# Performance work log

Hardware: AMD Instinct MI355X
Metric: run time of the kernel (lower is better)

## Reference

```python
import jax, jax.numpy as jnp
import numpy as np

D = 512
H = 8
DH = D // H
DFF = 2048
SLOTS = 1024
TOPK = 5
LN_EPS = 1e-5
NORM_EPS = 1e-12


def setup_inputs() -> dict:
    key = jax.random.key(0)
    ks = jax.random.split(key, 12)
    B, S = 8, 1024
    inp = {
        "src": jax.random.normal(ks[0], (B, S, D), dtype=jnp.float32),
        # MultiheadAttention params (torch layout: in_proj [3D, D], out_proj [D, D])
        "in_proj_w": jax.random.normal(ks[1], (3 * D, D), dtype=jnp.float32) * 0.02,
        "in_proj_b": jnp.zeros((3 * D,), dtype=jnp.float32),
        "out_proj_w": jax.random.normal(ks[2], (D, D), dtype=jnp.float32) * 0.02,
        "out_proj_b": jnp.zeros((D,), dtype=jnp.float32),
        # BPBookMemory params
        "memory": jax.random.normal(ks[3], (SLOTS, D), dtype=jnp.float32),
        "retrieval_scale": jnp.asarray(0.1, dtype=jnp.float32),
        # LayerNorms
        "ln1_g": jnp.ones((D,), dtype=jnp.float32),
        "ln1_b": jnp.zeros((D,), dtype=jnp.float32),
        "ln2_g": jnp.ones((D,), dtype=jnp.float32),
        "ln2_b": jnp.zeros((D,), dtype=jnp.float32),
        # FFN (torch Linear layout: [out, in])
        "w1": jax.random.normal(ks[4], (DFF, D), dtype=jnp.float32) * 0.02,
        "b1": jnp.zeros((DFF,), dtype=jnp.float32),
        "w2": jax.random.normal(ks[5], (D, DFF), dtype=jnp.float32) * 0.02,
        "b2": jnp.zeros((D,), dtype=jnp.float32),
    }
    return inp


def _layer_norm(x, g, b):
    mu = jnp.mean(x, axis=-1, keepdims=True)
    var = jnp.var(x, axis=-1, keepdims=True)
    return (x - mu) * jax.lax.rsqrt(var + LN_EPS) * g + b


def _l2_normalize(x):
    n = jnp.linalg.norm(x, axis=-1, keepdims=True)
    return x / jnp.maximum(n, NORM_EPS)


def _forward(src, in_proj_w, in_proj_b, out_proj_w, out_proj_b,
             memory, retrieval_scale, ln1_g, ln1_b, ln2_g, ln2_b,
             w1, b1, w2, b2):
    B, S, _ = src.shape
    # ---- pre-norm self-attention ----
    h = _layer_norm(src, ln1_g, ln1_b)
    qkv = h @ in_proj_w.T + in_proj_b            # [B,S,3D]
    q, k, v = jnp.split(qkv, 3, axis=-1)
    q = q.reshape(B, S, H, DH)
    k = k.reshape(B, S, H, DH)
    v = v.reshape(B, S, H, DH)
    scores = jnp.einsum("bqhd,bkhd->bhqk", q, k) / jnp.sqrt(jnp.float32(DH))
    attn = jax.nn.softmax(scores, axis=-1)
    ctx = jnp.einsum("bhqk,bkhd->bqhd", attn, v).reshape(B, S, D)
    attn_out = ctx @ out_proj_w.T + out_proj_b
    src = src + attn_out
    # ---- BP-Book memory: cosine sim -> topk -> softmax -> gather -> weighted sum ----
    xn = _l2_normalize(src)                      # [B,S,D]
    mn = _l2_normalize(memory)                   # [SLOTS,D]
    sim = xn @ mn.T                              # [B,S,SLOTS]
    topk_scores, topk_idx = jax.lax.top_k(sim, TOPK)
    w = jax.nn.softmax(topk_scores, axis=-1)     # [B,S,TOPK]
    retrieved = memory[topk_idx]                 # [B,S,TOPK,D]
    weighted = jnp.einsum("bskd,bsk->bsd", retrieved, w)
    src = src + retrieval_scale * weighted
    # ---- FFN ----
    h = _layer_norm(src, ln2_g, ln2_b)
    ffn = jax.nn.gelu(h @ w1.T + b1, approximate=False) @ w2.T + b2
    return src + ffn


def reference(src, in_proj_w, in_proj_b, out_proj_w, out_proj_b,
              memory, retrieval_scale, ln1_g, ln1_b, ln2_g, ln2_b,
              w1, b1, w2, b2):
    return _forward(src, in_proj_w, in_proj_b, out_proj_w, out_proj_b,
                    memory, retrieval_scale, ln1_g, ln1_b, ln2_g, ln2_b,
                    w1, b1, w2, b2)
```

## Files before the change

### kernel.cpp

```cpp
#include <hip/hip_runtime.h>
#include <math.h>

#define D_ 512
#define H_ 8
#define DFF_ 2048
#define SLOTS_ 1024
#define TOPK_ 5
#define NCAND_ 8
#define NTOK_ 8192
#define SEQ_ 1024
#define LN_EPS_ 1e-5f

typedef __attribute__((ext_vector_type(8))) short bf16x8;
typedef __attribute__((ext_vector_type(4))) float f32x4;
typedef __attribute__((ext_vector_type(4))) unsigned u32x4;
typedef unsigned short u16;

__device__ inline void split2(float x, unsigned short& hi, unsigned short& lo) {
    unsigned u = __builtin_bit_cast(unsigned, x);
    hi = (unsigned short)(u >> 16);
    float h = __builtin_bit_cast(float, u & 0xFFFF0000u);
    float rem = x - h;
    lo = (unsigned short)(__builtin_bit_cast(unsigned, rem) >> 16);
}

__device__ __forceinline__ void gld16(const void* g, void* l) {
    __builtin_amdgcn_global_load_lds(
        (const __attribute__((address_space(1))) void*)g,
        (__attribute__((address_space(3))) void*)l, 16, 0, 0);
}

__device__ __forceinline__ int SW7(int r) { return (r ^ (r >> 3)) & 7; }
__device__ __forceinline__ const bf16x8* frag(const unsigned short* p, int r, int c) {
    return (const bf16x8*)(p + r * 64 + ((c ^ SW7(r)) << 3));
}

__global__ __launch_bounds__(256) void prep_kernel(
    const float* __restrict__ inw, const float* __restrict__ outw,
    const float* __restrict__ w1, const float* __restrict__ w2,
    const float* __restrict__ mem, const float* __restrict__ src,
    const float* __restrict__ ln1g, const float* __restrict__ ln1b,
    u16* __restrict__ inwh, u16* __restrict__ inwl,
    u16* __restrict__ outwh, u16* __restrict__ outwl,
    u16* __restrict__ w1h, u16* __restrict__ w2h,
    float* __restrict__ mn, u16* __restrict__ mnh, u16* __restrict__ mnl,
    u16* __restrict__ hh, u16* __restrict__ hl)
{
    const int bid = blockIdx.x;
    const int t = threadIdx.x;
    if (bid < 3072) {
        const int i = (bid * 256 + t) * 4;
        const float* x;
        u16 *hhp, *llp;
        int base;
        if (i < 786432)       { x = inw;  hhp = inwh;  llp = inwl;  base = 0; }
        else if (i < 1048576) { x = outw; hhp = outwh; llp = outwl; base = 786432; }
        else if (i < 2097152) { x = w1;   hhp = w1h;   llp = nullptr; base = 1048576; }
        else                  { x = w2;   hhp = w2h;   llp = nullptr; base = 2097152; }
        const int j = i - base;
        const float4 v = *(const float4*)(x + j);
        const float vv[4] = {v.x, v.y, v.z, v.w};
        u16 h[4], l[4];
#pragma unroll
        for (int e = 0; e < 4; ++e) split2(vv[e], h[e], l[e]);
        hhp[j + 0] = h[0]; hhp[j + 1] = h[1]; hhp[j + 2] = h[2]; hhp[j + 3] = h[3];
        if (llp) { llp[j + 0] = l[0]; llp[j + 1] = l[1]; llp[j + 2] = l[2]; llp[j + 3] = l[3]; }
    } else if (bid < 3328) {
        const int row = (bid - 3072) * 4 + (t >> 6);
        const int lane = t & 63;
        float v[8];
        float ss = 0.0f;
#pragma unroll
        for (int j = 0; j < 8; ++j) {
            v[j] = mem[(size_t)row * D_ + j * 64 + lane];
            ss += v[j] * v[j];
        }
#pragma unroll
        for (int off = 32; off; off >>= 1) ss += __shfl_xor(ss, off);
        const float inv = 1.0f / fmaxf(sqrtf(ss), 1e-12f);
#pragma unroll
        for (int j = 0; j < 8; ++j) {
            const float y = v[j] * inv;
            mn[(size_t)row * D_ + j * 64 + lane] = y;
            u16 h, l;
            split2(y, h, l);
            mnh[(size_t)row * D_ + j * 64 + lane] = h;
            mnl[(size_t)row * D_ + j * 64 + lane] = l;
        }
    } else {
        const int row = bid - 3328;
        const float a = src[(size_t)row * D_ + t];
        const float b = src[(size_t)row * D_ + t + 256];
        float s = a + b;
        float ss = a * a + b * b;
#pragma unroll
        for (int off = 32; off; off >>= 1) {
            s += __shfl_xor(s, off);
            ss += __shfl_xor(ss, off);
        }
        __shared__ float rs[4], rss[4];
        if ((t & 63) == 0) { rs[t >> 6] = s; rss[t >> 6] = ss; }
        __syncthreads();
        s = rs[0] + rs[1] + rs[2] + rs[3];
        ss = rss[0] + rss[1] + rss[2] + rss[3];
        const float mu = s * (1.0f / D_);
        const float var = ss * (1.0f / D_) - mu * mu;
        const float r = rsqrtf(var + LN_EPS_);
        const float y0 = (a - mu) * r * ln1g[t] + ln1b[t];
        const float y1 = (b - mu) * r * ln1g[t + 256] + ln1b[t + 256];
        u16 h0, l0, h1, l1;
        split2(y0, h0, l0);
        split2(y1, h1, l1);
        hh[(size_t)row * D_ + t] = h0;
        hh[(size_t)row * D_ + t + 256] = h1;
        hl[(size_t)row * D_ + t] = l0;
        hl[(size_t)row * D_ + t + 256] = l1;
    }
}

enum { EP_QKV = 0, EP_OUTPROJ = 1, EP_SIM = 2, EP_FFN1 = 3, EP_FFN2 = 4 };

template <int SPLIT, int MODE>
__global__ __launch_bounds__(256) void gemm_mf(
    const unsigned short* __restrict__ Ahg, const unsigned short* __restrict__ Alg,
    const unsigned short* __restrict__ Bhg, const unsigned short* __restrict__ Blg,
    const float* __restrict__ bias, const float* __restrict__ res,
    float* __restrict__ C,
    unsigned short* __restrict__ Ch, unsigned short* __restrict__ Cl,
    int M, int N, int K)
{
    __shared__ __align__(16) unsigned short sm[(SPLIT == 3 ? 4 : 2) * 8192];
    unsigned short* Ah = sm;
    unsigned short* Al = sm + 8192;
    unsigned short* Bh = sm + (SPLIT == 3 ? 16384 : 8192);
    unsigned short* Bl = sm + 24576;

    const int tid = threadIdx.x;
    const int lane = tid & 63;
    const int w = tid >> 6;
    const int wr = w >> 1, wc = w & 1;
    const int g = lane >> 4, ln = lane & 15;
    const int m0 = blockIdx.x * 128, n0 = blockIdx.y * 128;
    const int lrow8 = lane >> 3, lchunk = lane & 7;

    const unsigned short* gsrc;
    unsigned short* lds;
    int rbase, rofs, nblk;
    if (SPLIT == 3) {
        nblk = 16; rofs = 0;
        if (w == 0)      { gsrc = Ahg; lds = Ah; rbase = m0; }
        else if (w == 1) { gsrc = Alg; lds = Al; rbase = m0; }
        else if (w == 2) { gsrc = Bhg; lds = Bh; rbase = n0; }
        else             { gsrc = Blg; lds = Bl; rbase = n0; }
    } else {
        nblk = 8; rofs = (w & 1) * 64;
        if (w < 2) { gsrc = Ahg; lds = Ah; rbase = m0; }
        else       { gsrc = Bhg; lds = Bh; rbase = n0; }
    }

    f32x4 acc[4][4];
#pragma unroll
    for (int i = 0; i < 4; ++i)
#pragma unroll
        for (int j = 0; j < 4; ++j) acc[i][j] = (f32x4){0.f, 0.f, 0.f, 0.f};

    for (int k0 = 0; k0 < K; k0 += 64) {
#pragma unroll
        for (int blk = 0; blk < nblk; ++blk) {
            const int row = rofs + blk * 8 + lrow8;
            const int sc = lchunk ^ SW7(row);
            gld16(gsrc + (size_t)(rbase + row) * K + k0 + sc * 8,
                  lds + (rofs + blk * 8) * 64);
        }
        __syncthreads();

#pragma unroll
        for (int ks = 0; ks < 2; ++ks) {
            bf16x8 a_h[4], a_l[4], b_h[4], b_l[4];
#pragma unroll
            for (int mi = 0; mi < 4; ++mi) {
                a_h[mi] = *frag(Ah, wr * 64 + mi * 16 + ln, ks * 4 + g);
                if (SPLIT == 3) a_l[mi] = *frag(Al, wr * 64 + mi * 16 + ln, ks * 4 + g);
            }
#pragma unroll
            for (int ni = 0; ni < 4; ++ni) {
                b_h[ni] = *frag(Bh, wc * 64 + ni * 16 + ln, ks * 4 + g);
                if (SPLIT == 3) b_l[ni] = *frag(Bl, wc * 64 + ni * 16 + ln, ks * 4 + g);
            }
#pragma unroll
            for (int mi = 0; mi < 4; ++mi)
#pragma unroll
                for (int ni = 0; ni < 4; ++ni) {
                    acc[mi][ni] = __builtin_amdgcn_mfma_f32_16x16x32_bf16(
                        a_h[mi], b_h[ni], acc[mi][ni], 0, 0, 0);
                    if (SPLIT == 3) {
                        acc[mi][ni] = __builtin_amdgcn_mfma_f32_16x16x32_bf16(
                            a_h[mi], b_l[ni], acc[mi][ni], 0, 0, 0);
                        acc[mi][ni] = __builtin_amdgcn_mfma_f32_16x16x32_bf16(
                            a_l[mi], b_h[ni], acc[mi][ni], 0, 0, 0);
                    }
                }
        }
        __syncthreads();
    }

#pragma unroll
    for (int mi = 0; mi < 4; ++mi) {
#pragma unroll
        for (int ni = 0; ni < 4; ++ni) {
            const int gn = n0 + wc * 64 + ni * 16 + ln;
            const float bz = (MODE == EP_SIM) ? 0.0f : bias[gn];
#pragma unroll
            for (int r2 = 0; r2 < 4; ++r2) {
                const int gm = m0 + wr * 64 + mi * 16 + g * 4 + r2;
                float v = acc[mi][ni][r2];
                if (MODE == EP_SIM) {
                    unsigned short h16, l16;
                    split2(v, h16, l16);
                    Ch[(size_t)gm * N + gn] = h16;
                } else if (MODE == EP_QKV) {
                    v += bz;
                    if (gn < D_) v *= 0.125f;
                    unsigned short h16, l16;
                    split2(v, h16, l16);
                    Ch[(size_t)gm * N + gn] = h16;
                    Cl[(size_t)gm * N + gn] = l16;
                } else if (MODE == EP_OUTPROJ) {
                    v += bz + res[(size_t)gm * N + gn];
                    C[(size_t)gm * N + gn] = v;
                    unsigned short h16, l16;
                    split2(v, h16, l16);
                    Ch[(size_t)gm * N + gn] = h16;
                } else if (MODE == EP_FFN1) {
                    v += bz;
                    v = 0.5f * v * (1.0f + erff(v * 0.70710678118654752f));
                    unsigned short h16, l16;
                    split2(v, h16, l16);
                    Ch[(size_t)gm * N + gn] = h16;
                } else {
                    v += bz + res[(size_t)gm * N + gn];
                    C[(size_t)gm * N + gn] = v;
                }
            }
        }
    }
}

__global__ __launch_bounds__(256, 2) void attn_kernel(
    const unsigned short* __restrict__ qkvh, const unsigned short* __restrict__ qkvl,
    unsigned short* __restrict__ ctxh, unsigned short* __restrict__ ctxl)
{
    const int id = blockIdx.x;
    const int bh = id & 63;
    const int qt = id >> 6;
    const int b = bh >> 3, h = bh & 7;
    const int tok0 = b * SEQ_ + qt * 128;
    const int kbase0 = b * SEQ_;
    const int tid = threadIdx.x;
    const int lane = tid & 63;
    const int w = tid >> 6;
    const int ln = lane & 15, g = lane >> 4;
    const int lrow8 = lane >> 3, lchunk = lane & 7;

    __shared__ __align__(16) unsigned char smb[65536];
    unsigned*       PP  = (unsigned*)smb;
    unsigned short* Qh  = (unsigned short*)smb;
    unsigned short* Ql  = (unsigned short*)(smb + 16384);
    unsigned short* Kh  = (unsigned short*)(smb + 32768);
    unsigned short* Kl  = (unsigned short*)(smb + 40960);
    unsigned short* Vth = (unsigned short*)(smb + 49152);
    unsigned short* Vtl = (unsigned short*)(smb + 57344);

    const int qoff = h * 64, koff = 512 + h * 64, voff = 1024 + h * 64;

#pragma unroll
    for (int blk = 0; blk < 4; ++blk) {
        const int row = w * 32 + blk * 8 + lrow8;
        const int sc = lchunk ^ SW7(row);
        gld16(qkvh + (size_t)(tok0 + row) * 1536 + qoff + sc * 8,
              Qh + (w * 32 + blk * 8) * 64);
        gld16(qkvl + (size_t)(tok0 + row) * 1536 + qoff + sc * 8,
              Ql + (w * 32 + blk * 8) * 64);
    }
    __syncthreads();
    bf16x8 qfh[2][2], qfl[2][2];
#pragma unroll
    for (int qi = 0; qi < 2; ++qi)
#pragma unroll
        for (int ks = 0; ks < 2; ++ks) {
            qfh[qi][ks] = *frag(Qh, w * 32 + qi * 16 + ln, ks * 4 + g);
            qfl[qi][ks] = *frag(Ql, w * 32 + qi * 16 + ln, ks * 4 + g);
        }
    __syncthreads();

    f32x4 o[4][2];
#pragma unroll
    for (int di = 0; di < 4; ++di)
#pragma unroll
        for (int qi = 0; qi < 2; ++qi) o[di][qi] = (f32x4){0.f, 0.f, 0.f, 0.f};
    float mrow2[2] = {-INFINITY, -INFINITY};
    float lrow2[2] = {0.f, 0.f};

    const int p2 = tid & 31, dc = tid >> 5;

    for (int kt = 0; kt < 16; ++kt) {
        const int kb2 = kbase0 + kt * 64;
#pragma unroll
        for (int blk = 0; blk < 2; ++blk) {
            const int row = w * 16 + blk * 8 + lrow8;
            const int sc = lchunk ^ SW7(row);
            gld16(qkvh + (size_t)(kb2 + row) * 1536 + koff + sc * 8,
                  Kh + (w * 16 + blk * 8) * 64);
            gld16(qkvl + (size_t)(kb2 + row) * 1536 + koff + sc * 8,
                  Kl + (w * 16 + blk * 8) * 64);
        }
        {
            const size_t b0 = (size_t)(kb2 + 2 * p2) * 1536 + voff + dc * 8;
            const bf16x8 h0 = *(const bf16x8*)(qkvh + b0);
            const bf16x8 h1 = *(const bf16x8*)(qkvh + b0 + 1536);
            const bf16x8 l0 = *(const bf16x8*)(qkvl + b0);
            const bf16x8 l1 = *(const bf16x8*)(qkvl + b0 + 1536);
#pragma unroll
            for (int j = 0; j < 8; ++j) {
                const int d = dc * 8 + j;
                const int idx = d * 64 + (((p2 >> 2) ^ SW7(d)) << 3) + ((p2 & 3) << 1);
                *(unsigned*)&Vth[idx] = (unsigned)(unsigned short)h0[j]
                                      | ((unsigned)(unsigned short)h1[j] << 16);
                *(unsigned*)&Vtl[idx] = (unsigned)(unsigned short)l0[j]
                                      | ((unsigned)(unsigned short)l1[j] << 16);
            }
        }
        __syncthreads();

        f32x4 s[4][2];
#pragma unroll
        for (int ki = 0; ki < 4; ++ki)
#pragma unroll
            for (int qi = 0; qi < 2; ++qi) s[ki][qi] = (f32x4){0.f, 0.f, 0.f, 0.f};
        __builtin_amdgcn_s_setprio(1);
#pragma unroll
        for (int ks = 0; ks < 2; ++ks) {
            bf16x8 kbh[4], kbl[4];
#pragma unroll
            for (int ki = 0; ki < 4; ++ki) {
                kbh[ki] = *frag(Kh, ki * 16 + ln, ks * 4 + g);
                kbl[ki] = *frag(Kl, ki * 16 + ln, ks * 4 + g);
            }
#pragma unroll
            for (int ki = 0; ki < 4; ++ki)
#pragma unroll
                for (int qi = 0; qi < 2; ++qi) {
                    s[ki][qi] = __builtin_amdgcn_mfma_f32_16x16x32_bf16(kbh[ki], qfh[qi][ks], s[ki][qi], 0, 0, 0);
                    s[ki][qi] = __builtin_amdgcn_mfma_f32_16x16x32_bf16(kbh[ki], qfl[qi][ks], s[ki][qi], 0, 0, 0);
                    s[ki][qi] = __builtin_amdgcn_mfma_f32_16x16x32_bf16(kbl[ki], qfh[qi][ks], s[ki][qi], 0, 0, 0);
                }
        }
        __builtin_amdgcn_s_setprio(0);

        float tm2[2], alpha2[2], psum2[2];
#pragma unroll
        for (int qi = 0; qi < 2; ++qi) {
            float m01 = fmaxf(fmaxf(s[0][qi][0], s[0][qi][1]), fmaxf(s[0][qi][2], s[0][qi][3]));
            float m23 = fmaxf(fmaxf(s[1][qi][0], s[1][qi][1]), fmaxf(s[1][qi][2], s[1][qi][3]));
            float m45 = fmaxf(fmaxf(s[2][qi][0], s[2][qi][1]), fmaxf(s[2][qi][2], s[2][qi][3]));
            float m67 = fmaxf(fmaxf(s[3][qi][0], s[3][qi][1]), fmaxf(s[3][qi][2], s[3][qi][3]));
            tm2[qi] = fmaxf(fmaxf(m01, m23), fmaxf(m45, m67));
        }
#pragma unroll
        for (int qi = 0; qi < 2; ++qi) {
            tm2[qi] = fmaxf(tm2[qi], __shfl_xor(tm2[qi], 16));
            tm2[qi] = fmaxf(tm2[qi], __shfl_xor(tm2[qi], 32));
            const float mnew = fmaxf(mrow2[qi], tm2[qi]);
            alpha2[qi] = __expf(mrow2[qi] - mnew);
            mrow2[qi] = mnew;
            psum2[qi] = 0.f;
        }
#pragma unroll
        for (int qi = 0; qi < 2; ++qi)
#pragma unroll
            for (int ki = 0; ki < 4; ++ki) {
                u32x4 pv;
#pragma unroll
                for (int r2 = 0; r2 < 4; ++r2) {
                    const float p = __expf(s[ki][qi][r2] - mrow2[qi]);
                    psum2[qi] += p;
                    unsigned short h16, l16;
                    split2(p, h16, l16);
                    pv[r2] = (unsigned)h16 | ((unsigned)l16 << 16);
                }
                *(u32x4*)&PP[(w * 32 + qi * 16 + ln) * 64 + (((ki * 4 + g) ^ (ln & 7)) << 2)] = pv;
            }
#pragma unroll
        for (int qi = 0; qi < 2; ++qi) {
            psum2[qi] += __shfl_xor(psum2[qi], 16);
            psum2[qi] += __shfl_xor(psum2[qi], 32);
            lrow2[qi] = lrow2[qi] * alpha2[qi] + psum2[qi];
        }
#pragma unroll
        for (int di = 0; di < 4; ++di)
#pragma unroll
            for (int qi = 0; qi < 2; ++qi)
#pragma unroll
                for (int r2 = 0; r2 < 4; ++r2)
                    o[di][qi][r2] *= alpha2[qi];

        __builtin_amdgcn_s_setprio(1);
#pragma unroll
        for (int ks = 0; ks < 2; ++ks) {
            bf16x8 pah[2], pal[2];
#pragma unroll
            for (int qi = 0; qi < 2; ++qi) {
                const unsigned* rowp = PP + (w * 32 + qi * 16 + ln) * 64;
                const int c0 = (2 * ks + (g >> 1)) * 4 + (g & 1) * 2;
                const u32x4 q0 = *(const u32x4*)(rowp + (((c0    ) ^ (ln & 7)) << 2));
                const u32x4 q1 = *(const u32x4*)(rowp + (((c0 + 1) ^ (ln & 7)) << 2));
                u32x4 hu, lu;
                hu[0] = __builtin_amdgcn_perm(q0[1], q0[0], 0x05040100u);
                hu[1] = __builtin_amdgcn_perm(q0[3], q0[2], 0x05040100u);
                hu[2] = __builtin_amdgcn_perm(q1[1], q1[0], 0x05040100u);
                hu[3] = __builtin_amdgcn_perm(q1[3], q1[2], 0x05040100u);
                lu[0] = __builtin_amdgcn_perm(q0[1], q0[0], 0x07060302u);
                lu[1] = __builtin_amdgcn_perm(q0[3], q0[2], 0x07060302u);
                lu[2] = __builtin_amdgcn_perm(q1[1], q1[0], 0x07060302u);
                lu[3] = __builtin_amdgcn_perm(q1[3], q1[2], 0x07060302u);
                pah[qi] = __builtin_bit_cast(bf16x8, hu);
                pal[qi] = __builtin_bit_cast(bf16x8, lu);
            }
            bf16x8 vbh[4], vbl[4];
#pragma unroll
            for (int di = 0; di < 4; ++di) {
                vbh[di] = *frag(Vth, di * 16 + ln, ks * 4 + g);
                vbl[di] = *frag(Vtl, di * 16 + ln, ks * 4 + g);
            }
#pragma unroll
            for (int di = 0; di < 4; ++di)
#pragma unroll
                for (int qi = 0; qi < 2; ++qi) {
                    o[di][qi] = __builtin_amdgcn_mfma_f32_16x16x32_bf16(vbh[di], pah[qi], o[di][qi], 0, 0, 0);
                    o[di][qi] = __builtin_amdgcn_mfma_f32_16x16x32_bf16(vbh[di], pal[qi], o[di][qi], 0, 0, 0);
                    o[di][qi] = __builtin_amdgcn_mfma_f32_16x16x32_bf16(vbl[di], pah[qi], o[di][qi], 0, 0, 0);
                }
        }
        __builtin_amdgcn_s_setprio(0);
        __syncthreads();
    }

#pragma unroll
    for (int di = 0; di < 4; ++di)
#pragma unroll
        for (int qi = 0; qi < 2; ++qi) {
            const float inv = 1.0f / lrow2[qi];
            u32x4 tv;
#pragma unroll
            for (int r2 = 0; r2 < 4; ++r2) {
                const float v = o[di][qi][r2] * inv;
                unsigned short h16, l16;
                split2(v, h16, l16);
                tv[r2] = (unsigned)h16 | ((unsigned)l16 << 16);
            }
            *(u32x4*)&PP[(w * 32 + qi * 16 + ln) * 64 + (((di * 4 + g) ^ (ln & 7)) << 2)] = tv;
        }
    __syncthreads();
    {
        const int qrow = lane >> 1, halfd = lane & 1;
        const unsigned* rowp = PP + (w * 32 + qrow) * 64;
        const size_t gbase = (size_t)(tok0 + w * 32 + qrow) * D_ + h * 64;
#pragma unroll
        for (int gi = 0; gi < 2; ++gi) {
            const int di = halfd * 2 + gi;
#pragma unroll
            for (int pr = 0; pr < 2; ++pr) {
                const int c = di * 4 + pr * 2;
                const u32x4 t0 = *(const u32x4*)(rowp + (((c    ) ^ (qrow & 7)) << 2));
                const u32x4 t1 = *(const u32x4*)(rowp + (((c + 1) ^ (qrow & 7)) << 2));
                u32x4 hv, lv;
                hv[0] = __builtin_amdgcn_perm(t0[1], t0[0], 0x05040100u);
                hv[1] = __builtin_amdgcn_perm(t0[3], t0[2], 0x05040100u);
                hv[2] = __builtin_amdgcn_perm(t1[1], t1[0], 0x05040100u);
                hv[3] = __builtin_amdgcn_perm(t1[3], t1[2], 0x05040100u);
                lv[0] = __builtin_amdgcn_perm(t0[1], t0[0], 0x07060302u);
                lv[1] = __builtin_amdgcn_perm(t0[3], t0[2], 0x07060302u);
                lv[2] = __builtin_amdgcn_perm(t1[1], t1[0], 0x07060302u);
                lv[3] = __builtin_amdgcn_perm(t1[3], t1[2], 0x07060302u);
                *(u32x4*)(ctxh + gbase + di * 16 + pr * 8) = hv;
                *(u32x4*)(ctxl + gbase + di * 16 + pr * 8) = lv;
            }
        }
    }
}

__global__ __launch_bounds__(256) void topk_kernel(
    const u16* __restrict__ sim, const float* __restrict__ src2,
    const float* __restrict__ mn, const float* __restrict__ mem,
    const float* __restrict__ rs_ptr, const float* __restrict__ g2,
    const float* __restrict__ b2, float* __restrict__ out,
    unsigned short* __restrict__ h2h)
{
    const int row = blockIdx.x * 4 + (threadIdx.x >> 6);
    const int lane = threadIdx.x & 63;
    float v[16];
#pragma unroll
    for (int j = 0; j < 16; ++j) {
        const unsigned sv = sim[(size_t)row * SLOTS_ + j * 64 + lane];
        v[j] = __builtin_bit_cast(float, sv << 16);
    }

    int ci[NCAND_];
#pragma unroll
    for (int t = 0; t < NCAND_; ++t) {
        float bv = -INFINITY;
        int bi = 0x7fffffff;
#pragma unroll
        for (int j = 0; j < 16; ++j) {
            const int idx = j * 64 + lane;
            if (v[j] > bv) { bv = v[j]; bi = idx; }
        }
#pragma unroll
        for (int off = 32; off; off >>= 1) {
            const float ov = __shfl_xor(bv, off);
            const int oi = __shfl_xor(bi, off);
            if (ov > bv || (ov == bv && oi < bi)) { bv = ov; bi = oi; }
        }
        ci[t] = bi;
#pragma unroll
        for (int j = 0; j < 16; ++j)
            if (j * 64 + lane == bi) v[j] = -INFINITY;
    }

    float x[8];
    float ss = 0.0f;
#pragma unroll
    for (int j = 0; j < 8; ++j) {
        x[j] = src2[(size_t)row * D_ + j * 64 + lane];
        ss += x[j] * x[j];
    }
#pragma unroll
    for (int off = 32; off; off >>= 1) ss += __shfl_xor(ss, off);
    const float invn = 1.0f / fmaxf(sqrtf(ss), 1e-12f);

    float rv[NCAND_];
#pragma unroll
    for (int t = 0; t < NCAND_; ++t) {
        const float* mrow = mn + (size_t)ci[t] * D_;
        float acc = 0.0f;
#pragma unroll
        for (int j = 0; j < 8; ++j)
            acc = fmaf(x[j], mrow[j * 64 + lane], acc);
#pragma unroll
        for (int off = 32; off; off >>= 1) acc += __shfl_xor(acc, off);
        rv[t] = acc * invn;
    }

    float wv[TOPK_];
    int wi[TOPK_];
    bool used[NCAND_];
#pragma unroll
    for (int t = 0; t < NCAND_; ++t) used[t] = false;
#pragma unroll
    for (int t = 0; t < TOPK_; ++t) {
        float bv = -INFINITY;
        int bi = 0x7fffffff, bu = 0;
#pragma unroll
        for (int u = 0; u < NCAND_; ++u) {
            if (!used[u] && (rv[u] > bv || (rv[u] == bv && ci[u] < bi))) {
                bv = rv[u]; bi = ci[u]; bu = u;
            }
        }
        used[bu] = true;
        wv[t] = bv;
        wi[t] = bi;
    }

    float m = wv[0];
#pragma unroll
    for (int t = 1; t < TOPK_; ++t) m = fmaxf(m, wv[t]);
    float w[TOPK_], ssum = 0.0f;
#pragma unroll
    for (int t = 0; t < TOPK_; ++t) { w[t] = __expf(wv[t] - m); ssum += w[t]; }
    const float scale = rs_ptr[0] / ssum;

    float y[8];
    float s_ = 0.f, ss2 = 0.f;
#pragma unroll
    for (int j = 0; j < 8; ++j) {
        const int d = j * 64 + lane;
        float acc = 0.0f;
#pragma unroll
        for (int t = 0; t < TOPK_; ++t)
            acc += w[t] * mem[(size_t)wi[t] * D_ + d];
        y[j] = x[j] + scale * acc;
        out[(size_t)row * D_ + d] = y[j];
        s_ += y[j];
        ss2 += y[j] * y[j];
    }
#pragma unroll
    for (int off = 32; off; off >>= 1) {
        s_ += __shfl_xor(s_, off);
        ss2 += __shfl_xor(ss2, off);
    }
    const float mu = s_ * (1.0f / D_);
    const float var = ss2 * (1.0f / D_) - mu * mu;
    const float r = rsqrtf(var + LN_EPS_);
#pragma unroll
    for (int j = 0; j < 8; ++j) {
        const int d = j * 64 + lane;
        const float h2 = (y[j] - mu) * r * g2[d] + b2[d];
        unsigned short h16, l16;
        split2(h2, h16, l16);
        h2h[(size_t)row * D_ + d] = h16;
    }
}

extern "C" void kernel_launch(void* const* d_in, const int* in_sizes, int n_in,
                              void* d_out, int out_size, void* d_ws, size_t ws_size,
                              hipStream_t stream)
{
    const float* src  = (const float*)d_in[0];
    const float* inw  = (const float*)d_in[1];
    const float* inb  = (const float*)d_in[2];
    const float* outw = (const float*)d_in[3];
    const float* outb = (const float*)d_in[4];
    const float* mem  = (const float*)d_in[5];
    const float* rs   = (const float*)d_in[6];
    const float* ln1g = (const float*)d_in[7];
    const float* ln1b = (const float*)d_in[8];
    const float* ln2g = (const float*)d_in[9];
    const float* ln2b = (const float*)d_in[10];
    const float* w1   = (const float*)d_in[11];
    const float* b1   = (const float*)d_in[12];
    const float* w2   = (const float*)d_in[13];
    const float* b2   = (const float*)d_in[14];
    float* out = (float*)d_out;
    char* ws = (char*)d_ws;
    const size_t MB = 1024ull * 1024ull;

    float* mn   = (float*)(ws + 0);
    u16* mnh    = (u16*)(ws + 2 * MB);
    u16* mnl    = (u16*)(ws + 3 * MB);
    u16* h2h    = (u16*)(ws + 4 * MB);
    u16* inwh   = (u16*)(ws + 4 * MB);
    u16* inwl   = (u16*)(ws + 5 * MB + 512 * 1024);
    u16* outwh  = (u16*)(ws + 7 * MB);
    u16* outwl  = (u16*)(ws + 7 * MB + 512 * 1024);
    u16* w1h    = (u16*)(ws + 77 * MB);
    u16* w2h    = (u16*)(ws + 79 * MB);
    u16* hh     = (u16*)(ws + 13 * MB);
    u16* hl     = (u16*)(ws + 21 * MB);
    u16* qkvh   = (u16*)(ws + 29 * MB);
    u16* qkvl   = (u16*)(ws + 53 * MB);
    u16* ctxh   = (u16*)(ws + 13 * MB);
    u16* ctxl   = (u16*)(ws + 21 * MB);
    u16* sim16  = (u16*)(ws + 13 * MB);
    float* src2 = (float*)(ws + 45 * MB);
    u16* src2h  = (u16*)(ws + 61 * MB);
    u16* Gbf    = (u16*)(ws + 29 * MB);

    prep_kernel<<<dim3(11520), dim3(256), 0, stream>>>(
        inw, outw, w1, w2, mem, src, ln1g, ln1b,
        inwh, inwl, outwh, outwl, w1h, w2h, mn, mnh, mnl, hh, hl);
    gemm_mf<3, EP_QKV><<<dim3(64, 12), dim3(256), 0, stream>>>(
        hh, hl, inwh, inwl, inb, nullptr, nullptr, qkvh, qkvl, NTOK_, 1536, 512);
    attn_kernel<<<dim3(512), dim3(256), 0, stream>>>(qkvh, qkvl, ctxh, ctxl);
    gemm_mf<3, EP_OUTPROJ><<<dim3(64, 4), dim3(256), 0, stream>>>(
        ctxh, ctxl, outwh, outwl, outb, src, src2, src2h, nullptr, NTOK_, 512, 512);
    gemm_mf<1, EP_SIM><<<dim3(64, 8), dim3(256), 0, stream>>>(
        src2h, nullptr, mnh, nullptr, nullptr, nullptr, nullptr, sim16, nullptr, NTOK_, 1024, 512);
    topk_kernel<<<dim3(2048), dim3(256), 0, stream>>>(
        sim16, src2, mn, mem, rs, ln2g, ln2b, out, h2h);
    gemm_mf<1, EP_FFN1><<<dim3(64, 16), dim3(256), 0, stream>>>(
        h2h, nullptr, w1h, nullptr, b1, nullptr, nullptr, Gbf, nullptr, NTOK_, 2048, 512);
    gemm_mf<1, EP_FFN2><<<dim3(64, 4), dim3(256), 0, stream>>>(
        Gbf, nullptr, w2h, nullptr, b2, out, out, nullptr, nullptr, NTOK_, 512, 2048);
}
```

Before: 279.3 us.

## Widen FFN1 GEMM tile, defer softmax rescaling, pack bf16 splits in attention

The GEMM template gains an NI parameter, and FFN1 now uses 128x256 tiles with a larger LDS buffer. This improves A-tile reuse and halves the block count. In attention, the online-softmax rescale of o and l is skipped unless some row max grows by more than 8 (a wave-wide vote), which avoids exp and multiply work on most tiles. The hi/lo bf16 split of P now uses packed v_cvt_pk_bf16_f32 instructions, which round rather than truncate the hi part. Risks are more accumulator registers (lower occupancy) in the wide GEMM and exp values up to e^8 in the deferred path.

```diff
diff --git a/kernel.cpp b/kernel.cpp
--- a/kernel.cpp
+++ b/kernel.cpp
@@ -120,7 +120,7 @@
 
 enum { EP_QKV = 0, EP_OUTPROJ = 1, EP_SIM = 2, EP_FFN1 = 3, EP_FFN2 = 4 };
 
-template <int SPLIT, int MODE>
+template <int SPLIT, int MODE, int NI>
 __global__ __launch_bounds__(256) void gemm_mf(
     const unsigned short* __restrict__ Ahg, const unsigned short* __restrict__ Alg,
     const unsigned short* __restrict__ Bhg, const unsigned short* __restrict__ Blg,
@@ -129,7 +129,7 @@
     unsigned short* __restrict__ Ch, unsigned short* __restrict__ Cl,
     int M, int N, int K)
 {
-    __shared__ __align__(16) unsigned short sm[(SPLIT == 3 ? 4 : 2) * 8192];
+    __shared__ __align__(16) unsigned short sm[(SPLIT == 3 ? 4 : (NI == 8 ? 3 : 2)) * 8192];
     unsigned short* Ah = sm;
     unsigned short* Al = sm + 8192;
     unsigned short* Bh = sm + (SPLIT == 3 ? 16384 : 8192);
@@ -140,7 +140,7 @@
     const int w = tid >> 6;
     const int wr = w >> 1, wc = w & 1;
     const int g = lane >> 4, ln = lane & 15;
-    const int m0 = blockIdx.x * 128, n0 = blockIdx.y * 128;
+    const int m0 = blockIdx.x * 128, n0 = blockIdx.y * (NI * 32);
     const int lrow8 = lane >> 3, lchunk = lane & 7;
 
     const unsigned short* gsrc;
@@ -152,17 +152,20 @@
         else if (w == 1) { gsrc = Alg; lds = Al; rbase = m0; }
         else if (w == 2) { gsrc = Bhg; lds = Bh; rbase = n0; }
         else             { gsrc = Blg; lds = Bl; rbase = n0; }
+    } else if (NI == 8) {
+        if (w < 2) { gsrc = Ahg; lds = Ah; rbase = m0; rofs = w * 64;         nblk = 8; }
+        else       { gsrc = Bhg; lds = Bh; rbase = n0; rofs = (w - 2) * 128;  nblk = 16; }
     } else {
         nblk = 8; rofs = (w & 1) * 64;
         if (w < 2) { gsrc = Ahg; lds = Ah; rbase = m0; }
         else       { gsrc = Bhg; lds = Bh; rbase = n0; }
     }
 
-    f32x4 acc[4][4];
+    f32x4 acc[4][NI];
 #pragma unroll
     for (int i = 0; i < 4; ++i)
 #pragma unroll
-        for (int j = 0; j < 4; ++j) acc[i][j] = (f32x4){0.f, 0.f, 0.f, 0.f};
+        for (int j = 0; j < NI; ++j) acc[i][j] = (f32x4){0.f, 0.f, 0.f, 0.f};
 
     for (int k0 = 0; k0 < K; k0 += 64) {
 #pragma unroll
@@ -176,21 +179,21 @@
 
 #pragma unroll
         for (int ks = 0; ks < 2; ++ks) {
-            bf16x8 a_h[4], a_l[4], b_h[4], b_l[4];
+            bf16x8 a_h[4], a_l[4], b_h[NI], b_l[NI];
 #pragma unroll
             for (int mi = 0; mi < 4; ++mi) {
                 a_h[mi] = *frag(Ah, wr * 64 + mi * 16 + ln, ks * 4 + g);
                 if (SPLIT == 3) a_l[mi] = *frag(Al, wr * 64 + mi * 16 + ln, ks * 4 + g);
             }
 #pragma unroll
-            for (int ni = 0; ni < 4; ++ni) {
-                b_h[ni] = *frag(Bh, wc * 64 + ni * 16 + ln, ks * 4 + g);
-                if (SPLIT == 3) b_l[ni] = *frag(Bl, wc * 64 + ni * 16 + ln, ks * 4 + g);
+            for (int ni = 0; ni < NI; ++ni) {
+                b_h[ni] = *frag(Bh, wc * (NI * 16) + ni * 16 + ln, ks * 4 + g);
+                if (SPLIT == 3) b_l[ni] = *frag(Bl, wc * (NI * 16) + ni * 16 + ln, ks * 4 + g);
             }
 #pragma unroll
             for (int mi = 0; mi < 4; ++mi)
 #pragma unroll
-                for (int ni = 0; ni < 4; ++ni) {
+                for (int ni = 0; ni < NI; ++ni) {
                     acc[mi][ni] = __builtin_amdgcn_mfma_f32_16x16x32_bf16(
                         a_h[mi], b_h[ni], acc[mi][ni], 0, 0, 0);
                     if (SPLIT == 3) {
@@ -207,8 +210,8 @@
 #pragma unroll
     for (int mi = 0; mi < 4; ++mi) {
 #pragma unroll
-        for (int ni = 0; ni < 4; ++ni) {
-            const int gn = n0 + wc * 64 + ni * 16 + ln;
+        for (int ni = 0; ni < NI; ++ni) {
+            const int gn = n0 + wc * (NI * 16) + ni * 16 + ln;
             const float bz = (MODE == EP_SIM) ? 0.0f : bias[gn];
 #pragma unroll
             for (int r2 = 0; r2 < 4; ++r2) {
@@ -357,7 +360,7 @@
         }
         __builtin_amdgcn_s_setprio(0);
 
-        float tm2[2], alpha2[2], psum2[2];
+        float tm2[2], psum2[2];
 #pragma unroll
         for (int qi = 0; qi < 2; ++qi) {
             float m01 = fmaxf(fmaxf(s[0][qi][0], s[0][qi][1]), fmaxf(s[0][qi][2], s[0][qi][3]));
@@ -365,44 +368,61 @@
             float m45 = fmaxf(fmaxf(s[2][qi][0], s[2][qi][1]), fmaxf(s[2][qi][2], s[2][qi][3]));
             float m67 = fmaxf(fmaxf(s[3][qi][0], s[3][qi][1]), fmaxf(s[3][qi][2], s[3][qi][3]));
             tm2[qi] = fmaxf(fmaxf(m01, m23), fmaxf(m45, m67));
-        }
-#pragma unroll
-        for (int qi = 0; qi < 2; ++qi) {
             tm2[qi] = fmaxf(tm2[qi], __shfl_xor(tm2[qi], 16));
             tm2[qi] = fmaxf(tm2[qi], __shfl_xor(tm2[qi], 32));
-            const float mnew = fmaxf(mrow2[qi], tm2[qi]);
-            alpha2[qi] = __expf(mrow2[qi] - mnew);
-            mrow2[qi] = mnew;
             psum2[qi] = 0.f;
         }
+        const int defer = __all((tm2[0] <= mrow2[0] + 8.0f) &&
+                                (tm2[1] <= mrow2[1] + 8.0f));
+        if (!defer) {
+            float alpha2[2];
+#pragma unroll
+            for (int qi = 0; qi < 2; ++qi) {
+                const float mnew = fmaxf(mrow2[qi], tm2[qi]);
+                alpha2[qi] = __expf(mrow2[qi] - mnew);
+                mrow2[qi] = mnew;
+                lrow2[qi] *= alpha2[qi];
+            }
+#pragma unroll
+            for (int di = 0; di < 4; ++di)
+#pragma unroll
+                for (int qi = 0; qi < 2; ++qi)
+#pragma unroll
+                    for (int r2 = 0; r2 < 4; ++r2)
+                        o[di][qi][r2] *= alpha2[qi];
+        }
 #pragma unroll
         for (int qi = 0; qi < 2; ++qi)
 #pragma unroll
             for (int ki = 0; ki < 4; ++ki) {
+                const float p0 = __expf(s[ki][qi][0] - mrow2[qi]);
+                const float p1 = __expf(s[ki][qi][1] - mrow2[qi]);
+                const float p2v = __expf(s[ki][qi][2] - mrow2[qi]);
+                const float p3 = __expf(s[ki][qi][3] - mrow2[qi]);
+                psum2[qi] += (p0 + p1) + (p2v + p3);
+                unsigned hp01, hp23, lp01, lp23;
+                asm("v_cvt_pk_bf16_f32 %0, %1, %2" : "=v"(hp01) : "v"(p0), "v"(p1));
+                asm("v_cvt_pk_bf16_f32 %0, %1, %2" : "=v"(hp23) : "v"(p2v), "v"(p3));
+                const float h0 = __builtin_bit_cast(float, hp01 << 16);
+                const float h1 = __builtin_bit_cast(float, hp01 & 0xFFFF0000u);
+                const float h2 = __builtin_bit_cast(float, hp23 << 16);
+                const float h3 = __builtin_bit_cast(float, hp23 & 0xFFFF0000u);
+                const float r0 = p0 - h0, r1 = p1 - h1, r2f = p2v - h2, r3 = p3 - h3;
+                asm("v_cvt_pk_bf16_f32 %0, %1, %2" : "=v"(lp01) : "v"(r0), "v"(r1));
+                asm("v_cvt_pk_bf16_f32 %0, %1, %2" : "=v"(lp23) : "v"(r2f), "v"(r3));
                 u32x4 pv;
-#pragma unroll
-                for (int r2 = 0; r2 < 4; ++r2) {
-                    const float p = __expf(s[ki][qi][r2] - mrow2[qi]);
-                    psum2[qi] += p;
-                    unsigned short h16, l16;
-                    split2(p, h16, l16);
-                    pv[r2] = (unsigned)h16 | ((unsigned)l16 << 16);
-                }
+                pv[0] = __builtin_amdgcn_perm(lp01, hp01, 0x05040100u);
+                pv[1] = __builtin_amdgcn_perm(lp01, hp01, 0x07060302u);
+                pv[2] = __builtin_amdgcn_perm(lp23, hp23, 0x05040100u);
+                pv[3] = __builtin_amdgcn_perm(lp23, hp23, 0x07060302u);
                 *(u32x4*)&PP[(w * 32 + qi * 16 + ln) * 64 + (((ki * 4 + g) ^ (ln & 7)) << 2)] = pv;
             }
 #pragma unroll
         for (int qi = 0; qi < 2; ++qi) {
             psum2[qi] += __shfl_xor(psum2[qi], 16);
             psum2[qi] += __shfl_xor(psum2[qi], 32);
-            lrow2[qi] = lrow2[qi] * alpha2[qi] + psum2[qi];
-        }
-#pragma unroll
-        for (int di = 0; di < 4; ++di)
-#pragma unroll
-            for (int qi = 0; qi < 2; ++qi)
-#pragma unroll
-                for (int r2 = 0; r2 < 4; ++r2)
-                    o[di][qi][r2] *= alpha2[qi];
+            lrow2[qi] += psum2[qi];
+        }
 
         __builtin_amdgcn_s_setprio(1);
 #pragma unroll
@@ -658,17 +678,17 @@
     prep_kernel<<<dim3(11520), dim3(256), 0, stream>>>(
         inw, outw, w1, w2, mem, src, ln1g, ln1b,
         inwh, inwl, outwh, outwl, w1h, w2h, mn, mnh, mnl, hh, hl);
-    gemm_mf<3, EP_QKV><<<dim3(64, 12), dim3(256), 0, stream>>>(
+    gemm_mf<3, EP_QKV, 4><<<dim3(64, 12), dim3(256), 0, stream>>>(
         hh, hl, inwh, inwl, inb, nullptr, nullptr, qkvh, qkvl, NTOK_, 1536, 512);
     attn_kernel<<<dim3(512), dim3(256), 0, stream>>>(qkvh, qkvl, ctxh, ctxl);
-    gemm_mf<3, EP_OUTPROJ><<<dim3(64, 4), dim3(256), 0, stream>>>(
+    gemm_mf<3, EP_OUTPROJ, 4><<<dim3(64, 4), dim3(256), 0, stream>>>(
         ctxh, ctxl, outwh, outwl, outb, src, src2, src2h, nullptr, NTOK_, 512, 512);
-    gemm_mf<1, EP_SIM><<<dim3(64, 8), dim3(256), 0, stream>>>(
+    gemm_mf<1, EP_SIM, 4><<<dim3(64, 8), dim3(256), 0, stream>>>(
         src2h, nullptr, mnh, nullptr, nullptr, nullptr, nullptr, sim16, nullptr, NTOK_, 1024, 512);
     topk_kernel<<<dim3(2048), dim3(256), 0, stream>>>(
         sim16, src2, mn, mem, rs, ln2g, ln2b, out, h2h);
-    gemm_mf<1, EP_FFN1><<<dim3(64, 16), dim3(256), 0, stream>>>(
+    gemm_mf<1, EP_FFN1, 8><<<dim3(64, 8), dim3(256), 0, stream>>>(
         h2h, nullptr, w1h, nullptr, b1, nullptr, nullptr, Gbf, nullptr, NTOK_, 2048, 512);
-    gemm_mf<1, EP_FFN2><<<dim3(64, 4), dim3(256), 0, stream>>>(
+    gemm_mf<1, EP_FFN2, 4><<<dim3(64, 4), dim3(256), 0, stream>>>(
         Gbf, nullptr, w2h, nullptr, b2, out, out, nullptr, nullptr, NTOK_, 512, 2048);
 }
```

New measurement: 302.2 us. +8.2%, slower.
